# Kernel tuning notes

Hardware: AMD Instinct MI355X
Metric: run time of the kernel (lower is better)

The kernel has to match this reference:

```python
import jax, jax.numpy as jnp
import numpy as np

B, N, D, R = 2, 256, 128, 32

def _sh_l1(r):
    # e3nn-style component-normalized l=1 spherical harmonics of unit vectors
    return jnp.sqrt(3.0) * r

def _sh_l2(r):
    x, y, z = r[..., 0], r[..., 1], r[..., 2]
    c = jnp.sqrt(15.0)
    return jnp.stack([
        c * x * y,
        c * y * z,
        0.5 * jnp.sqrt(5.0) * (3.0 * z * z - 1.0),  # x^2+y^2+z^2 = 1
        c * x * z,
        0.5 * c * (x * x - y * y),
    ], axis=-1)

def _radial(rbf, w1, b1, w2, b2):
    h = rbf @ w1 + b1
    return (h * jax.nn.sigmoid(h)) @ w2 + b2  # Linear -> SiLU -> Linear

def _layernorm(x, g, b, eps=1e-5):
    m = jnp.mean(x, axis=-1, keepdims=True)
    v = jnp.var(x, axis=-1, keepdims=True)
    return (x - m) * jax.lax.rsqrt(v + eps) * g + b

def setup_inputs() -> dict:
    key = jax.random.key(0)
    ks = iter(jax.random.split(key, 40))
    def nrm(shape, s=1.0):
        return jax.random.normal(next(ks), shape, dtype=jnp.float32) * s
    r_hat = nrm((B, N, N, 3))
    r_hat = r_hat / (jnp.linalg.norm(r_hat, axis=-1, keepdims=True) + 1e-9)
    inp = {
        'node_s': nrm((B, N, D)),
        'node_v': nrm((B, N, 3, D)),
        'node_t': nrm((B, N, 5, D)),
        'rbf': jax.random.uniform(next(ks), (B, N, N, R), dtype=jnp.float32),
        'r_hat': r_hat,
        'mask': jnp.ones((B, N, N), dtype=jnp.float32),
    }
    s1, s2 = 1.0 / np.sqrt(R), 1.0 / np.sqrt(D)
    for p in ('r0', 'r1', 'r2', 'r110'):
        inp[p + '_w1'] = nrm((R, D), s1)
        inp[p + '_b1'] = jnp.zeros((D,), jnp.float32)
        inp[p + '_w2'] = nrm((D, D), s2)
        inp[p + '_b2'] = jnp.zeros((D,), jnp.float32)
    inp['src_w'] = nrm((D, D), s2)
    inp['ln_g'] = jnp.ones((D,), jnp.float32)
    inp['ln_b'] = jnp.zeros((D,), jnp.float32)
    inp['out_w'] = nrm((D, D), s2)
    inp['out_b'] = jnp.zeros((D,), jnp.float32)
    inp['v_scale'] = jnp.ones((D,), jnp.float32)
    inp['t_scale'] = jnp.ones((D,), jnp.float32)
    return inp

def reference(node_s, node_v, node_t, rbf, r_hat, mask,
              r0_w1, r0_b1, r0_w2, r0_b2,
              r1_w1, r1_b1, r1_w2, r1_b2,
              r2_w1, r2_b1, r2_w2, r2_b2,
              r110_w1, r110_b1, r110_w2, r110_b2,
              src_w, ln_g, ln_b, out_w, out_b, v_scale, t_scale):
    h = node_s @ src_w                               # (B,N,D)
    h_j = h[:, None, :, :] * mask[..., None]         # (B,N,N,D): h_j[b,i,j]=h[b,j]*mask[b,i,j]
    Y1 = _sh_l1(r_hat)                               # (B,N,N,3)
    Y2 = _sh_l2(r_hat)                               # (B,N,N,5)

    msg_s = jnp.sum(h_j * _radial(rbf, r0_w1, r0_b1, r0_w2, r0_b2), axis=2)  # (B,N,D)
    delta_v = jnp.einsum('bijd,bijc->bicd',
                         h_j * _radial(rbf, r1_w1, r1_b1, r1_w2, r1_b2), Y1) * v_scale
    delta_t = jnp.einsum('bijd,bijc->bicd',
                         h_j * _radial(rbf, r2_w1, r2_b1, r2_w2, r2_b2), Y2) * t_scale

    # v_j[b,i,j] = node_v[b,i] (per the torch unsqueeze(2).expand)
    dot_vY1 = jnp.einsum('bicd,bijc->bijd', node_v, Y1)                      # (B,N,N,D)
    msg_s_from_v = jnp.sum(dot_vY1 * _radial(rbf, r110_w1, r110_b1, r110_w2, r110_b2)
                           * mask[..., None], axis=2)                        # (B,N,D)

    delta_s = _layernorm(msg_s + msg_s_from_v, ln_g, ln_b) @ out_w + out_b
    return (delta_s, delta_v, delta_t)
```

## Files before the change

### kernel.cpp

```cpp
#include <hip/hip_runtime.h>

#define Bb 2
#define Nn 256
#define Dd 128
#define Rr 32

typedef unsigned short u16;
typedef unsigned int   u32;
typedef __attribute__((ext_vector_type(8))) short bf16x8;
typedef __attribute__((ext_vector_type(4))) short bf16x4;
typedef __attribute__((ext_vector_type(4))) float f32x4;
typedef __attribute__((ext_vector_type(2))) u32   u32x2;
typedef __attribute__((ext_vector_type(4))) u32   u32x4;

__device__ u16 g_w1t[4*Dd*Rr];
__device__ u16 g_w2t[4*Dd*Dd];

__device__ __forceinline__ short f2bfs(float f){
  u32 u = __float_as_uint(f);
  u += 0x7FFFu + ((u >> 16) & 1u);
  return (short)(u >> 16);
}
__device__ __forceinline__ u16 f2bf(float f){
  u32 u = __float_as_uint(f);
  u += 0x7FFFu + ((u >> 16) & 1u);
  return (u16)(u >> 16);
}
__device__ __forceinline__ u32 cvtpk(float a, float b){
  u32 r;
  asm("v_cvt_pk_bf16_f32 %0, %1, %2" : "=v"(r) : "v"(a), "v"(b));
  return r;
}
__device__ __forceinline__ int swz(int j){
  return (j&3) | ((((j>>2)^(j>>3))&1)<<2);
}

__global__ __launch_bounds__(128) void prep_kernel(
    const float* __restrict__ node_s, const float* __restrict__ src_w,
    const float* __restrict__ r0w1, const float* __restrict__ r1w1,
    const float* __restrict__ r2w1, const float* __restrict__ r3w1,
    const float* __restrict__ r0w2, const float* __restrict__ r1w2,
    const float* __restrict__ r2w2, const float* __restrict__ r3w2,
    float* __restrict__ h_out)
{
  const int bx = blockIdx.x;
  const int t  = threadIdx.x;
  if (bx < Bb*Nn){
    __shared__ float s_row[Dd];
    s_row[t] = node_s[(size_t)bx*Dd + t];
    __syncthreads();
    float acc = 0.f;
    #pragma unroll 8
    for (int k=0;k<Dd;k++) acc += s_row[k]*src_w[k*Dd + t];
    h_out[(size_t)bx*Dd + t] = acc;
  } else {
    const int kb = bx - Bb*Nn;
    const int p  = kb >> 3, sl = kb & 7;
    const float* W1 = (p==0)?r0w1:(p==1)?r1w1:(p==2)?r2w1:r3w1;
    const float* W2 = (p==0)?r0w2:(p==1)?r1w2:(p==2)?r2w2:r3w2;
    u16* W1T = g_w1t + p*Dd*Rr;
    u16* W2T = g_w2t + p*Dd*Dd;
    #pragma unroll
    for (int it=0; it<4; it++){
      int in = sl*512 + it*128 + t;
      W1T[(in & 127)*Rr + (in >> 7)] = f2bf(W1[in]);
    }
    #pragma unroll
    for (int it=0; it<16; it++){
      int in = sl*2048 + it*128 + t;
      W2T[(in & 127)*Dd + (in >> 7)] = f2bf(W2[in]);
    }
  }
}

__global__ __launch_bounds__(512,2) void se3_mfma11(
    const float* __restrict__ node_v,
    const float* __restrict__ rbf,
    const float* __restrict__ r_hat,
    const float* __restrict__ maskp,
    const float* __restrict__ r0b1, const float* __restrict__ r0b2,
    const float* __restrict__ r1b1, const float* __restrict__ r1b2,
    const float* __restrict__ r2b1, const float* __restrict__ r2b2,
    const float* __restrict__ r3b1, const float* __restrict__ r3b2,
    const float* __restrict__ ln_g, const float* __restrict__ ln_b,
    const float* __restrict__ out_w, const float* __restrict__ out_b,
    const float* __restrict__ v_scale, const float* __restrict__ t_scale,
    const float* __restrict__ h_ws,
    float* __restrict__ out_s, float* __restrict__ out_v, float* __restrict__ out_t)
{
  __shared__ u16   s_rbf[Nn*36];
  __shared__ u16   s_hid[2*64*128];
  __shared__ u16   s_YT[10*264];
  __shared__ u16   s_Y1r[3*264];
  __shared__ float s_red[16*130];
  __shared__ float s_msg[Dd];
  __shared__ float s_xn[Dd];
  __shared__ float s_part[4*Dd];
  __shared__ float s_mv[2];

  const int tid  = threadIdx.x;
  const int bi   = blockIdx.x;
  const int b    = bi >> 8;
  const int lane = tid & 63;
  const int w    = tid >> 6;
  const int q    = lane >> 4;
  const int cc   = lane & 15;
  const int mpair= w & 1;
  const int dgrp = w >> 1;
  const int dbase= dgrp*32;

  if (tid < Nn){
    int j = tid;
    size_t pidx = (size_t)bi*Nn + j;
    float mk = maskp[pidx];
    float x = r_hat[pidx*3+0];
    float y = r_hat[pidx*3+1];
    float z = r_hat[pidx*3+2];
    const float SQ3=1.7320508075688772f;
    const float C15=3.8729833462074170f;
    const float C5H=1.1180339887498949f;
    float y1a=SQ3*x, y1b=SQ3*y, y1c=SQ3*z;
    s_YT[0*264+j]=f2bf(mk);
    s_YT[1*264+j]=f2bf(y1a*mk);
    s_YT[2*264+j]=f2bf(y1b*mk);
    s_YT[3*264+j]=f2bf(y1c*mk);
    s_YT[4*264+j]=f2bf(C15*x*y*mk);
    s_YT[5*264+j]=f2bf(C15*y*z*mk);
    s_YT[6*264+j]=f2bf(C5H*(3.f*z*z-1.f)*mk);
    s_YT[7*264+j]=f2bf(C15*x*z*mk);
    s_YT[8*264+j]=f2bf(0.5f*C15*(x*x-y*y)*mk);
    s_YT[9*264+j]=f2bf(mk);
    s_Y1r[0*264+j]=f2bf(y1a);
    s_Y1r[1*264+j]=f2bf(y1b);
    s_Y1r[2*264+j]=f2bf(y1c);
  }

  const float* rbf_blk = rbf + (size_t)bi*Nn*Rr;
  const float* hb      = h_ws + (size_t)b*Nn*Dd;

  for (int idx=tid; idx<Nn*Rr/2; idx+=512){
    int j = idx >> 4, r2 = (idx & 15)*2;
    const float* src = &rbf_blk[j*Rr + r2];
    float v0 = src[0], v1 = src[1];
    *(u32*)&s_rbf[j*36 + r2] = cvtpk(v0, v1);
  }

  bf16x8 vBf[2];
  {
    const float* nv = node_v + (size_t)bi*3*Dd;
    #pragma unroll
    for (int nt=0;nt<2;nt++){
      int dd = dbase+nt*16+cc;
      bf16x8 t = {0,0,0,0,0,0,0,0};
      if (q==0){
        t[0]=f2bfs(nv[0*Dd+dd]);
        t[1]=f2bfs(nv[1*Dd+dd]);
        t[2]=f2bfs(nv[2*Dd+dd]);
      }
      vBf[nt]=t;
    }
  }

  __syncthreads();

  const f32x4 zf = {0.f,0.f,0.f,0.f};
  f32x4 accred[2] = {zf, zf};
  int buf = 0;

  #pragma unroll 1
  for (int p=0;p<4;p++){
    const float* B1p = (p==0)?r0b1:(p==1)?r1b1:(p==2)?r2b1:r3b1;
    const float* B2p = (p==0)?r0b2:(p==1)?r1b2:(p==2)?r2b2:r3b2;
    const u16* W1T = g_w1t + p*Dd*Rr;
    const u16* W2T = g_w2t + p*Dd*Dd;
    const int lo = (p==0)?0:(p==1)?1:(p==2)?4:9;
    const int hi = (p==0)?0:(p==1)?3:(p==2)?8:9;
    const u32 gmask = (cc>=lo && cc<=hi) ? 0xFFFFFFFFu : 0u;
    const u16* ytrow = &s_YT[(cc<10?cc:9)*264];

    bf16x8 w1f[2];
    bf16x8 w2f[2][4];
    f32x4  b1v4[2];
    float  b2v[2];
    #pragma unroll
    for (int nt=0;nt<2;nt++){
      int dd = dbase+nt*16+cc;
      b1v4[nt] = *(const f32x4*)&B1p[dbase + nt*16 + q*4];
      b2v[nt]=B2p[dd];
      w1f[nt] = *(const bf16x8*)&W1T[dd*Rr + q*8];
      #pragma unroll
      for (int ks=0;ks<4;ks++)
        w2f[nt][ks] = *(const bf16x8*)&W2T[dd*Dd + ks*32 + q*8];
    }

    #pragma unroll 1
    for (int ch=0; ch<4; ch++){
      #pragma unroll
      for (int jt=0;jt<2;jt++){
        const int jrow = (mpair*2+jt)*16 + cc;
        const u16* bp = &s_rbf[(ch*64 + jrow)*36 + q*8];
        bf16x4 lo4 = *(const bf16x4*)bp;
        bf16x4 hi4 = *(const bf16x4*)(bp+4);
        bf16x8 rbff = {lo4[0],lo4[1],lo4[2],lo4[3],hi4[0],hi4[1],hi4[2],hi4[3]};
        #pragma unroll
        for (int nt=0;nt<2;nt++){
          f32x4 hc = __builtin_amdgcn_mfma_f32_16x16x32_bf16(w1f[nt], rbff, zf, 0,0,0);
          float s[4];
          #pragma unroll
          for (int r=0;r<4;r++){
            float x  = hc[r] + b1v4[nt][r];
            float e  = __expf(-x);
            s[r]     = x*__builtin_amdgcn_rcpf(1.f+e);
          }
          u32x2 pk = { cvtpk(s[0], s[1]), cvtpk(s[2], s[3]) };
          const int c0 = dgrp*4 + nt*2 + (q>>1);
          *(u32x2*)&s_hid[buf*8192 + jrow*128 + ((c0 ^ swz(jrow))<<3) + (q&1)*4] = pk;
        }
      }
      __syncthreads();

      u32 bB[2][4];
      #pragma unroll
      for (int mm=0;mm<2;mm++){
        const int jp = mpair*32 + ((cc>>2)<<3) + mm*4 + (cc&3);
        bf16x8 af[4];
        #pragma unroll
        for (int ks=0;ks<4;ks++)
          af[ks] = *(const bf16x8*)&s_hid[buf*8192 + jp*128 + (((ks*4+q) ^ swz(jp))<<3)];

        f32x4 dotC[2];
        if (p==3){
          bf16x8 aY = {0,0,0,0,0,0,0,0};
          if (q==0){
            int jg = ch*64 + jp;
            aY[0]=(short)s_Y1r[0*264+jg];
            aY[1]=(short)s_Y1r[1*264+jg];
            aY[2]=(short)s_Y1r[2*264+jg];
          }
          #pragma unroll
          for (int nt=0;nt<2;nt++)
            dotC[nt] = __builtin_amdgcn_mfma_f32_16x16x32_bf16(aY, vBf[nt], zf, 0,0,0);
        }

        #pragma unroll
        for (int nt=0;nt<2;nt++){
          f32x4 c2 = zf;
          #pragma unroll
          for (int ks=0;ks<4;ks++)
            c2 = __builtin_amdgcn_mfma_f32_16x16x32_bf16(af[ks], w2f[nt][ks], c2, 0,0,0);
          const int dd = dbase+nt*16+cc;
          float g[4];
          if (p<3){
            const float* hp = hb + (size_t)(ch*64 + mpair*32 + q*8 + mm*4)*Dd + dd;
            #pragma unroll
            for (int r=0;r<4;r++)
              g[r] = (c2[r]+b2v[nt]) * hp[(size_t)r*Dd];
          } else {
            #pragma unroll
            for (int r=0;r<4;r++)
              g[r] = (c2[r]+b2v[nt]) * dotC[nt][r];
          }
          bB[nt][mm*2+0] = cvtpk(g[0], g[1]);
          bB[nt][mm*2+1] = cvtpk(g[2], g[3]);
        }
      }

      {
        bf16x8 aR = *(const bf16x8*)(ytrow + ch*64 + mpair*32 + q*8);
        u32* arp = (u32*)&aR;
        arp[0]&=gmask; arp[1]&=gmask; arp[2]&=gmask; arp[3]&=gmask;
        #pragma unroll
        for (int nt=0;nt<2;nt++){
          u32x4 bw = { bB[nt][0], bB[nt][1], bB[nt][2], bB[nt][3] };
          bf16x8 bG = __builtin_bit_cast(bf16x8, bw);
          accred[nt] = __builtin_amdgcn_mfma_f32_16x16x32_bf16(aR, bG, accred[nt], 0,0,0);
        }
      }
      buf ^= 1;
    }
  }

  if (mpair){
    #pragma unroll
    for (int nt=0;nt<2;nt++){
      const int d = dbase + nt*16 + cc;
      #pragma unroll
      for (int r=0;r<4;r++)
        s_red[(q*4+r)*130 + d] = accred[nt][r];
    }
  }
  __syncthreads();
  if (!mpair){
    #pragma unroll
    for (int nt=0;nt<2;nt++){
      const int d = dbase + nt*16 + cc;
      #pragma unroll
      for (int r=0;r<4;r++){
        const int rw = q*4 + r;
        float val = accred[nt][r] + s_red[rw*130 + d];
        if (rw==0)      s_msg[d] = val;
        else if (rw<=3) out_v[(size_t)bi*3*Dd + (size_t)(rw-1)*Dd + d] = val*v_scale[d];
        else if (rw<=8) out_t[(size_t)bi*5*Dd + (size_t)(rw-4)*Dd + d] = val*t_scale[d];
        else if (rw==9) s_xn[d] = val;
      }
    }
  }
  __syncthreads();

  if (tid < 64){
    float a0=s_msg[tid]+s_xn[tid], a1=s_msg[tid+64]+s_xn[tid+64];
    float s1=a0+a1, s2=a0*a0+a1*a1;
    #pragma unroll
    for (int off=1;off<64;off<<=1){
      s1 += __shfl_xor(s1,off);
      s2 += __shfl_xor(s2,off);
    }
    if (tid==0){
      float m   = s1*(1.f/Dd);
      float var = fmaxf(s2*(1.f/Dd) - m*m, 0.f);
      s_mv[0]=m;
      s_mv[1]=rsqrtf(var+1e-5f);
    }
  }
  __syncthreads();
  if (tid < Dd){
    float msg = s_msg[tid]+s_xn[tid];
    s_xn[tid] = (msg - s_mv[0])*s_mv[1]*ln_g[tid] + ln_b[tid];
  }
  __syncthreads();

  {
    int dp = tid & 127, seg = tid >> 7;
    float pa = 0.f;
    #pragma unroll 8
    for (int k=seg*32;k<seg*32+32;k++)
      pa += s_xn[k]*out_w[k*Dd+dp];
    s_part[seg*Dd+dp]=pa;
  }
  __syncthreads();
  if (tid < Dd)
    out_s[(size_t)bi*Dd+tid] = s_part[tid]+s_part[Dd+tid]+s_part[2*Dd+tid]+s_part[3*Dd+tid]+out_b[tid];
}

extern "C" void kernel_launch(void* const* d_in, const int* in_sizes, int n_in,
                              void* d_out, int out_size, void* d_ws, size_t ws_size,
                              hipStream_t stream) {
  const float* node_s = (const float*)d_in[0];
  const float* node_v = (const float*)d_in[1];
  const float* rbf    = (const float*)d_in[3];
  const float* r_hat  = (const float*)d_in[4];
  const float* maskp  = (const float*)d_in[5];
  const float* r0w1=(const float*)d_in[6],  *r0b1=(const float*)d_in[7];
  const float* r0w2=(const float*)d_in[8],  *r0b2=(const float*)d_in[9];
  const float* r1w1=(const float*)d_in[10], *r1b1=(const float*)d_in[11];
  const float* r1w2=(const float*)d_in[12], *r1b2=(const float*)d_in[13];
  const float* r2w1=(const float*)d_in[14], *r2b1=(const float*)d_in[15];
  const float* r2w2=(const float*)d_in[16], *r2b2=(const float*)d_in[17];
  const float* r3w1=(const float*)d_in[18], *r3b1=(const float*)d_in[19];
  const float* r3w2=(const float*)d_in[20], *r3b2=(const float*)d_in[21];
  const float* src_w  =(const float*)d_in[22];
  const float* ln_g   =(const float*)d_in[23];
  const float* ln_b   =(const float*)d_in[24];
  const float* out_w  =(const float*)d_in[25];
  const float* out_b  =(const float*)d_in[26];
  const float* v_scale=(const float*)d_in[27];
  const float* t_scale=(const float*)d_in[28];

  float* h_ws = (float*)d_ws;
  float* out_s = (float*)d_out;
  float* out_v = out_s + (size_t)Bb*Nn*Dd;
  float* out_t = out_v + (size_t)Bb*Nn*3*Dd;

  prep_kernel<<<dim3(Bb*Nn + 32), dim3(128), 0, stream>>>(
      node_s, src_w,
      r0w1, r1w1, r2w1, r3w1, r0w2, r1w2, r2w2, r3w2,
      h_ws);
  se3_mfma11<<<dim3(Bb*Nn), dim3(512), 0, stream>>>(
      node_v, rbf, r_hat, maskp,
      r0b1,r0b2, r1b1,r1b2, r2b1,r2b2, r3b1,r3b2,
      ln_g, ln_b, out_w, out_b, v_scale, t_scale,
      h_ws, out_s, out_v, out_t);
}
```

Before: 203.3 us.

## Repartition work so each wave owns 16 channels across all j rows

Each of the 8 waves now owns a 16-wide slice of the D dimension and handles all 64 j rows per chunk, instead of a 32-wide slice over half the rows. This removes the cross-wave accumulator reduction through shared memory and one barrier, and halves the per-wave weight fragments held in registers. Launch bounds rise to 4 blocks per SM to raise occupancy, and several inner loops are no longer unrolled to keep register use low. The cost is more serialized MFMA chains per wave and less instruction-level parallelism.

```diff
diff --git a/kernel.cpp b/kernel.cpp
--- a/kernel.cpp
+++ b/kernel.cpp
@@ -73,7 +73,7 @@
   }
 }
 
-__global__ __launch_bounds__(512,2) void se3_mfma11(
+__global__ __launch_bounds__(512,4) void se3_mfma12(
     const float* __restrict__ node_v,
     const float* __restrict__ rbf,
     const float* __restrict__ r_hat,
@@ -92,7 +92,6 @@
   __shared__ u16   s_hid[2*64*128];
   __shared__ u16   s_YT[10*264];
   __shared__ u16   s_Y1r[3*264];
-  __shared__ float s_red[16*130];
   __shared__ float s_msg[Dd];
   __shared__ float s_xn[Dd];
   __shared__ float s_part[4*Dd];
@@ -105,9 +104,7 @@
   const int w    = tid >> 6;
   const int q    = lane >> 4;
   const int cc   = lane & 15;
-  const int mpair= w & 1;
-  const int dgrp = w >> 1;
-  const int dbase= dgrp*32;
+  const int dwb  = w*16;
 
   if (tid < Nn){
     int j = tid;
@@ -145,26 +142,23 @@
     *(u32*)&s_rbf[j*36 + r2] = cvtpk(v0, v1);
   }
 
-  bf16x8 vBf[2];
+  bf16x8 vBf;
   {
     const float* nv = node_v + (size_t)bi*3*Dd;
-    #pragma unroll
-    for (int nt=0;nt<2;nt++){
-      int dd = dbase+nt*16+cc;
-      bf16x8 t = {0,0,0,0,0,0,0,0};
-      if (q==0){
-        t[0]=f2bfs(nv[0*Dd+dd]);
-        t[1]=f2bfs(nv[1*Dd+dd]);
-        t[2]=f2bfs(nv[2*Dd+dd]);
-      }
-      vBf[nt]=t;
-    }
+    int dd = dwb+cc;
+    bf16x8 t = {0,0,0,0,0,0,0,0};
+    if (q==0){
+      t[0]=f2bfs(nv[0*Dd+dd]);
+      t[1]=f2bfs(nv[1*Dd+dd]);
+      t[2]=f2bfs(nv[2*Dd+dd]);
+    }
+    vBf=t;
   }
 
   __syncthreads();
 
   const f32x4 zf = {0.f,0.f,0.f,0.f};
-  f32x4 accred[2] = {zf, zf};
+  f32x4 accred = zf;
   int buf = 0;
 
   #pragma unroll 1
@@ -178,131 +172,100 @@
     const u32 gmask = (cc>=lo && cc<=hi) ? 0xFFFFFFFFu : 0u;
     const u16* ytrow = &s_YT[(cc<10?cc:9)*264];
 
-    bf16x8 w1f[2];
-    bf16x8 w2f[2][4];
-    f32x4  b1v4[2];
-    float  b2v[2];
-    #pragma unroll
-    for (int nt=0;nt<2;nt++){
-      int dd = dbase+nt*16+cc;
-      b1v4[nt] = *(const f32x4*)&B1p[dbase + nt*16 + q*4];
-      b2v[nt]=B2p[dd];
-      w1f[nt] = *(const bf16x8*)&W1T[dd*Rr + q*8];
-      #pragma unroll
-      for (int ks=0;ks<4;ks++)
-        w2f[nt][ks] = *(const bf16x8*)&W2T[dd*Dd + ks*32 + q*8];
-    }
+    bf16x8 w1f  = *(const bf16x8*)&W1T[(dwb+cc)*Rr + q*8];
+    bf16x8 w2f[4];
+    #pragma unroll
+    for (int ks=0;ks<4;ks++)
+      w2f[ks] = *(const bf16x8*)&W2T[(dwb+cc)*Dd + ks*32 + q*8];
+    f32x4 b1v4 = *(const f32x4*)&B1p[dwb + q*4];
+    float b2v  = B2p[dwb + cc];
 
     #pragma unroll 1
     for (int ch=0; ch<4; ch++){
-      #pragma unroll
-      for (int jt=0;jt<2;jt++){
-        const int jrow = (mpair*2+jt)*16 + cc;
+      #pragma unroll 1
+      for (int jt=0;jt<4;jt++){
+        const int jrow = jt*16 + cc;
         const u16* bp = &s_rbf[(ch*64 + jrow)*36 + q*8];
         bf16x4 lo4 = *(const bf16x4*)bp;
         bf16x4 hi4 = *(const bf16x4*)(bp+4);
         bf16x8 rbff = {lo4[0],lo4[1],lo4[2],lo4[3],hi4[0],hi4[1],hi4[2],hi4[3]};
+        f32x4 hc = __builtin_amdgcn_mfma_f32_16x16x32_bf16(w1f, rbff, zf, 0,0,0);
+        float s[4];
         #pragma unroll
-        for (int nt=0;nt<2;nt++){
-          f32x4 hc = __builtin_amdgcn_mfma_f32_16x16x32_bf16(w1f[nt], rbff, zf, 0,0,0);
-          float s[4];
-          #pragma unroll
-          for (int r=0;r<4;r++){
-            float x  = hc[r] + b1v4[nt][r];
-            float e  = __expf(-x);
-            s[r]     = x*__builtin_amdgcn_rcpf(1.f+e);
-          }
-          u32x2 pk = { cvtpk(s[0], s[1]), cvtpk(s[2], s[3]) };
-          const int c0 = dgrp*4 + nt*2 + (q>>1);
-          *(u32x2*)&s_hid[buf*8192 + jrow*128 + ((c0 ^ swz(jrow))<<3) + (q&1)*4] = pk;
+        for (int r=0;r<4;r++){
+          float x  = hc[r] + b1v4[r];
+          float e  = __expf(-x);
+          s[r]     = x*__builtin_amdgcn_rcpf(1.f+e);
         }
+        u32x2 pk = { cvtpk(s[0], s[1]), cvtpk(s[2], s[3]) };
+        const int c0 = w*2 + (q>>1);
+        *(u32x2*)&s_hid[buf*8192 + jrow*128 + ((c0 ^ swz(jrow))<<3) + (q&1)*4] = pk;
       }
       __syncthreads();
 
-      u32 bB[2][4];
-      #pragma unroll
-      for (int mm=0;mm<2;mm++){
-        const int jp = mpair*32 + ((cc>>2)<<3) + mm*4 + (cc&3);
-        bf16x8 af[4];
-        #pragma unroll
-        for (int ks=0;ks<4;ks++)
-          af[ks] = *(const bf16x8*)&s_hid[buf*8192 + jp*128 + (((ks*4+q) ^ swz(jp))<<3)];
-
-        f32x4 dotC[2];
-        if (p==3){
-          bf16x8 aY = {0,0,0,0,0,0,0,0};
-          if (q==0){
-            int jg = ch*64 + jp;
-            aY[0]=(short)s_Y1r[0*264+jg];
-            aY[1]=(short)s_Y1r[1*264+jg];
-            aY[2]=(short)s_Y1r[2*264+jg];
+      #pragma unroll 1
+      for (int g=0; g<2; g++){
+        u32 bB[4];
+        #pragma unroll 1
+        for (int mm=0;mm<2;mm++){
+          const int jp = g*32 + ((cc>>2)<<3) + mm*4 + (cc&3);
+          bf16x8 af[4];
+          #pragma unroll
+          for (int ks=0;ks<4;ks++)
+            af[ks] = *(const bf16x8*)&s_hid[buf*8192 + jp*128 + (((ks*4+q) ^ swz(jp))<<3)];
+
+          f32x4 dotC;
+          if (p==3){
+            bf16x8 aY = {0,0,0,0,0,0,0,0};
+            if (q==0){
+              int jg = ch*64 + jp;
+              aY[0]=(short)s_Y1r[0*264+jg];
+              aY[1]=(short)s_Y1r[1*264+jg];
+              aY[2]=(short)s_Y1r[2*264+jg];
+            }
+            dotC = __builtin_amdgcn_mfma_f32_16x16x32_bf16(aY, vBf, zf, 0,0,0);
           }
-          #pragma unroll
-          for (int nt=0;nt<2;nt++)
-            dotC[nt] = __builtin_amdgcn_mfma_f32_16x16x32_bf16(aY, vBf[nt], zf, 0,0,0);
-        }
-
-        #pragma unroll
-        for (int nt=0;nt<2;nt++){
+
           f32x4 c2 = zf;
           #pragma unroll
           for (int ks=0;ks<4;ks++)
-            c2 = __builtin_amdgcn_mfma_f32_16x16x32_bf16(af[ks], w2f[nt][ks], c2, 0,0,0);
-          const int dd = dbase+nt*16+cc;
-          float g[4];
+            c2 = __builtin_amdgcn_mfma_f32_16x16x32_bf16(af[ks], w2f[ks], c2, 0,0,0);
+          const int dd = dwb+cc;
+          float gg[4];
           if (p<3){
-            const float* hp = hb + (size_t)(ch*64 + mpair*32 + q*8 + mm*4)*Dd + dd;
+            const float* hp = hb + (size_t)(ch*64 + g*32 + q*8 + mm*4)*Dd + dd;
             #pragma unroll
             for (int r=0;r<4;r++)
-              g[r] = (c2[r]+b2v[nt]) * hp[(size_t)r*Dd];
+              gg[r] = (c2[r]+b2v) * hp[(size_t)r*Dd];
           } else {
             #pragma unroll
             for (int r=0;r<4;r++)
-              g[r] = (c2[r]+b2v[nt]) * dotC[nt][r];
+              gg[r] = (c2[r]+b2v) * dotC[r];
           }
-          bB[nt][mm*2+0] = cvtpk(g[0], g[1]);
-          bB[nt][mm*2+1] = cvtpk(g[2], g[3]);
+          bB[mm*2+0] = cvtpk(gg[0], gg[1]);
+          bB[mm*2+1] = cvtpk(gg[2], gg[3]);
         }
-      }
-
-      {
-        bf16x8 aR = *(const bf16x8*)(ytrow + ch*64 + mpair*32 + q*8);
+        bf16x8 aR = *(const bf16x8*)(ytrow + ch*64 + g*32 + q*8);
         u32* arp = (u32*)&aR;
         arp[0]&=gmask; arp[1]&=gmask; arp[2]&=gmask; arp[3]&=gmask;
-        #pragma unroll
-        for (int nt=0;nt<2;nt++){
-          u32x4 bw = { bB[nt][0], bB[nt][1], bB[nt][2], bB[nt][3] };
-          bf16x8 bG = __builtin_bit_cast(bf16x8, bw);
-          accred[nt] = __builtin_amdgcn_mfma_f32_16x16x32_bf16(aR, bG, accred[nt], 0,0,0);
-        }
+        u32x4 bw = { bB[0], bB[1], bB[2], bB[3] };
+        bf16x8 bG = __builtin_bit_cast(bf16x8, bw);
+        accred = __builtin_amdgcn_mfma_f32_16x16x32_bf16(aR, bG, accred, 0,0,0);
       }
       buf ^= 1;
     }
   }
 
-  if (mpair){
-    #pragma unroll
-    for (int nt=0;nt<2;nt++){
-      const int d = dbase + nt*16 + cc;
-      #pragma unroll
-      for (int r=0;r<4;r++)
-        s_red[(q*4+r)*130 + d] = accred[nt][r];
-    }
-  }
-  __syncthreads();
-  if (!mpair){
-    #pragma unroll
-    for (int nt=0;nt<2;nt++){
-      const int d = dbase + nt*16 + cc;
-      #pragma unroll
-      for (int r=0;r<4;r++){
-        const int rw = q*4 + r;
-        float val = accred[nt][r] + s_red[rw*130 + d];
-        if (rw==0)      s_msg[d] = val;
-        else if (rw<=3) out_v[(size_t)bi*3*Dd + (size_t)(rw-1)*Dd + d] = val*v_scale[d];
-        else if (rw<=8) out_t[(size_t)bi*5*Dd + (size_t)(rw-4)*Dd + d] = val*t_scale[d];
-        else if (rw==9) s_xn[d] = val;
-      }
+  {
+    const int d = dwb + cc;
+    #pragma unroll
+    for (int r=0;r<4;r++){
+      const int rw = q*4 + r;
+      float val = accred[r];
+      if (rw==0)      s_msg[d] = val;
+      else if (rw<=3) out_v[(size_t)bi*3*Dd + (size_t)(rw-1)*Dd + d] = val*v_scale[d];
+      else if (rw<=8) out_t[(size_t)bi*5*Dd + (size_t)(rw-4)*Dd + d] = val*t_scale[d];
+      else if (rw==9) s_xn[d] = val;
     }
   }
   __syncthreads();
@@ -375,7 +338,7 @@
       node_s, src_w,
       r0w1, r1w1, r2w1, r3w1, r0w2, r1w2, r2w2, r3w2,
       h_ws);
-  se3_mfma11<<<dim3(Bb*Nn), dim3(512), 0, stream>>>(
+  se3_mfma12<<<dim3(Bb*Nn), dim3(512), 0, stream>>>(
       node_v, rbf, r_hat, maskp,
       r0b1,r0b2, r1b1,r1b2, r2b1,r2b2, r3b1,r3b2,
       ln_g, ln_b, out_w, out_b, v_scale, t_scale,
```

Result: faster. 187.9 us (-7.6%).
